# Performance work log

Measured on AMD Instinct MI355X. Metric: run time of the kernel, lower is better.

The kernel has to match this reference:

```python
import jax, jax.numpy as jnp
import numpy as np

SR = 24000          # sampling_rate
HARM = 8            # harmonic_num
DIM = HARM + 1
SINE_AMP = 0.1
NOISE_STD = 0.003
VTHR = 0.0          # voiced_threshold


def setup_inputs() -> dict:
    key = jax.random.key(0)
    k1, k2, k3, k4 = jax.random.split(key, 4)
    B, T, UPP = 16, 800, 256
    f0 = jax.random.uniform(k1, (B, T), minval=0.0, maxval=400.0)
    f0 = f0 * (jax.random.uniform(k2, (B, T)) > 0.2).astype(jnp.float32)
    rand_ini = jax.random.uniform(k3, (B, DIM)).at[:, 0].set(0.0)
    noise_z = jax.random.normal(k4, (B, T * UPP, DIM), dtype=jnp.float32)
    return {"f0": f0, "rand_ini": rand_ini, "noise_z": noise_z, "upp": UPP}


def _linear_interp_align_corners(x, upp):
    # x: [B, T, D] -> [B, T*upp, D], matches F.interpolate(mode='linear', align_corners=True)
    B, T, D = x.shape
    L = T * upp
    pos = jnp.arange(L, dtype=x.dtype) * (T - 1) / (L - 1)
    i0 = jnp.clip(jnp.floor(pos).astype(jnp.int32), 0, T - 2)
    frac = (pos - i0.astype(x.dtype))[None, :, None]
    x0 = jnp.take(x, i0, axis=1)
    x1 = jnp.take(x, i0 + 1, axis=1)
    return x0 + frac * (x1 - x0)


def reference(f0, rand_ini, noise_z, upp):
    B, T = f0.shape
    dt = f0.dtype
    # harmonic stack: f0_buf[:, :, k] = f0 * (k+1)
    harmonics = jnp.arange(1, DIM + 1, dtype=dt)
    f0_buf = f0[:, :, None] * harmonics                      # [B, T, DIM]
    rad = (f0_buf / SR) % 1.0                                # normalized phase increments
    rad = rad.at[:, 0, :].add(rand_ini)                      # random initial phase (col 0 fixed)
    # phase-wrap detection via upsampled cumulative phase
    tmp = jnp.cumsum(rad, axis=1) * upp
    tmp = _linear_interp_align_corners(tmp, upp)             # [B, L, DIM]
    rad_up = jnp.repeat(rad, upp, axis=1)                    # nearest upsample [B, L, DIM]
    tmp = tmp % 1.0
    wrap = (tmp[:, 1:, :] - tmp[:, :-1, :]) < 0
    shift = jnp.concatenate(
        [jnp.zeros((B, 1, DIM), dt), -wrap.astype(dt)], axis=1
    )
    sine_waves = jnp.sin(jnp.cumsum(rad_up + shift, axis=1) * (2.0 * np.pi)) * SINE_AMP
    # voiced/unvoiced mask, nearest upsampled
    uv = (f0 > VTHR).astype(dt)[:, :, None]                  # [B, T, 1]
    uv = jnp.repeat(uv, upp, axis=1)                         # [B, L, 1]
    noise_amp = uv * NOISE_STD + (1.0 - uv) * (SINE_AMP / 3.0)
    noise = noise_amp * noise_z
    sine_waves = sine_waves * uv + noise
    return (sine_waves, uv, noise)
```

## Files before the change

kernel.cpp:

```cpp
#include <hip/hip_runtime.h>

#define DIMH 9
#define FR8 8

typedef float f4 __attribute__((ext_vector_type(4)));
typedef float f2 __attribute__((ext_vector_type(2)));

__global__ __launch_bounds__(256) void scan_kernel(
    const float* __restrict__ f0, const float* __restrict__ rand_ini,
    float* __restrict__ Pf, int B, int T, int upp)
{
    int bk = blockIdx.x;
    int b = bk / DIMH;
    int k = bk - b * DIMH;
    int tid = threadIdx.x;
    float hk = (float)(k + 1);

    int t0 = tid * 4;
    f4 fv = {0.f, 0.f, 0.f, 0.f};
    if (t0 < T) fv = *(const f4*)(f0 + (size_t)b * T + t0);

    double s[4];
    double run = 0.0;
    #pragma unroll
    for (int j = 0; j < 4; ++j) {
        float x = fv[j] * hk * (1.0f / 24000.0f);
        float rad = x - truncf(x);
        if (t0 == 0 && j == 0) rad += rand_ini[b * DIMH + k];
        run += (double)rad;
        s[j] = run;
    }

    double tot = run;
    int lane = tid & 63;
    #pragma unroll
    for (int d = 1; d < 64; d <<= 1) {
        double u = __shfl_up(tot, d);
        if (lane >= d) tot += u;
    }
    __shared__ double wsum[4];
    int wid = tid >> 6;
    if (lane == 63) wsum[wid] = tot;
    __syncthreads();
    double excl = tot - run;
    for (int w = 0; w < wid; ++w) excl += wsum[w];

    if (t0 < T) {
        f4 o;
        double du = (double)upp;
        #pragma unroll
        for (int j = 0; j < 4; ++j) {
            double up = (excl + s[j]) * du;
            o[j] = (float)(up - (double)(long long)up);
        }
        *(f4*)(Pf + ((size_t)bk) * (size_t)T + t0) = o;
    }
}

template <int UPP>
__global__ __launch_bounds__(512) void sine_kernel_t(
    const float* __restrict__ f0, const float* __restrict__ rand_ini,
    const float* __restrict__ noise_z, const float* __restrict__ Pf,
    float* __restrict__ out, int B, int T)
{
    int nfb = T / FR8;
    int gb = blockIdx.x;
    int b = gb / nfb;
    int t0 = (gb - b * nfb) * FR8;
    int tid = threadIdx.x;

    __shared__ f2 srp[FR8 * DIMH];
    __shared__ float suv[FR8], snamp[FR8];

    if (tid < FR8 * DIMH) {
        int tl = tid / DIMH;
        int k  = tid - tl * DIMH;
        int t  = t0 + tl;
        float f0v = f0[(size_t)b * T + t];
        float x = f0v * (float)(k + 1) * (1.0f / 24000.0f);
        float rad = x - truncf(x);
        if (t == 0) rad += rand_ini[b * DIMH + k];
        f2 v;
        v.x = rad;
        v.y = (t > 0) ? Pf[((size_t)b * DIMH + k) * T + (t - 1)] : 0.0f;
        srp[tid] = v;
        if (k == 0) {
            float uv = (f0v > 0.0f) ? 1.0f : 0.0f;
            suv[tl] = uv;
            snamp[tl] = uv * 0.003f + (1.0f - uv) * (0.1f / 3.0f);
        }
    }
    __syncthreads();

    size_t L = (size_t)T * (size_t)UPP;
    float* out_sine  = out;
    float* out_uv    = out + (size_t)B * L * DIMH;
    float* out_noise = out_uv + (size_t)B * L;

    {
        int f = tid >> 6;
        float u = suv[f];
        f4 uvv = {u, u, u, u};
        f4* uvp = (f4*)(out_uv + (size_t)b * L + (size_t)t0 * UPP);
        uvp[tid] = uvv;
    }

    size_t base = ((size_t)b * L + (size_t)t0 * UPP) * DIMH;
    const f4* nzp = (const f4*)(noise_z + base);
    f4* sp = (f4*)(out_sine + base);
    f4* np = (f4*)(out_noise + base);

    constexpr int NIT = FR8 * UPP * DIMH / 4 / 512;
    #pragma unroll
    for (int it = 0; it < NIT; ++it) {
        int v  = tid + it * 512;
        int e0 = v << 2;
        int s  = e0 / DIMH;
        int k  = e0 - s * DIMH;
        int fidx = s / UPP;
        int rr   = s - fidx * UPP;
        float uv   = suv[fidx];
        float namp = snamp[fidx];
        f4 nz = __builtin_nontemporal_load(nzp + v);
        f4 sv, nov;
        #pragma unroll
        for (int j = 0; j < 4; ++j) {
            f2 rp = srp[fidx * DIMH + k];
            float C  = fmaf((float)(rr + 1), rp.x, rp.y);
            float fr = C - truncf(C);
#if __has_builtin(__builtin_amdgcn_sinf)
            float sn = __builtin_amdgcn_sinf(fr) * 0.1f;
#else
            float sn = sinf(6.283185307179586f * fr) * 0.1f;
#endif
            float no = namp * nz[j];
            sv[j]  = fmaf(sn, uv, no);
            nov[j] = no;
            if (++k == DIMH) { k = 0; ++rr; }
        }
        sp[v] = sv;
        np[v] = nov;
    }
}

__global__ __launch_bounds__(256) void sine_kernel_rt(
    const float* __restrict__ f0, const float* __restrict__ rand_ini,
    const float* __restrict__ noise_z, const float* __restrict__ Pf,
    float* __restrict__ out, int B, int T, int upp)
{
    const int FRAMES = 4;
    int nfb = T / FRAMES;
    int gb = blockIdx.x;
    int b = gb / nfb;
    int t0 = (gb - b * nfb) * FRAMES;
    int tid = threadIdx.x;

    __shared__ f2 srp[4 * DIMH];
    __shared__ float suv[4], snamp[4];

    if (tid < FRAMES * DIMH) {
        int tl = tid / DIMH;
        int k  = tid - tl * DIMH;
        int t  = t0 + tl;
        float f0v = f0[(size_t)b * T + t];
        float x = f0v * (float)(k + 1) * (1.0f / 24000.0f);
        float rad = x - truncf(x);
        if (t == 0) rad += rand_ini[b * DIMH + k];
        f2 v; v.x = rad;
        v.y = (t > 0) ? Pf[((size_t)b * DIMH + k) * T + (t - 1)] : 0.0f;
        srp[tid] = v;
        if (k == 0) {
            float uv = (f0v > 0.0f) ? 1.0f : 0.0f;
            suv[tl] = uv;
            snamp[tl] = uv * 0.003f + (1.0f - uv) * (0.1f / 3.0f);
        }
    }
    __syncthreads();

    size_t L = (size_t)T * (size_t)upp;
    float* out_sine  = out;
    float* out_uv    = out + (size_t)B * L * DIMH;
    float* out_noise = out_uv + (size_t)B * L;

    for (int i = tid; i < FRAMES * upp / 4; i += 256) {
        int f = i / (upp >> 2);
        float u = suv[f];
        f4 uvv = {u, u, u, u};
        ((f4*)(out_uv + (size_t)b * L + (size_t)t0 * upp))[i] = uvv;
    }

    size_t base = ((size_t)b * L + (size_t)t0 * upp) * DIMH;
    const f4* nzp = (const f4*)(noise_z + base);
    f4* sp = (f4*)(out_sine + base);
    f4* np = (f4*)(out_noise + base);

    int totf4 = FRAMES * upp * DIMH / 4;
    for (int v = tid; v < totf4; v += 256) {
        int e0 = v << 2;
        int s  = e0 / DIMH;
        int k  = e0 - s * DIMH;
        int fidx = s / upp;
        int rr   = s - fidx * upp;
        float uv   = suv[fidx];
        float namp = snamp[fidx];
        f4 nz = nzp[v];
        f4 sv, nov;
        #pragma unroll
        for (int j = 0; j < 4; ++j) {
            f2 rp = srp[fidx * DIMH + k];
            float C  = fmaf((float)(rr + 1), rp.x, rp.y);
            float fr = C - truncf(C);
            float sn = sinf(6.283185307179586f * fr) * 0.1f;
            float no = namp * nz[j];
            sv[j]  = fmaf(sn, uv, no);
            nov[j] = no;
            if (++k == DIMH) { k = 0; ++rr; }
        }
        sp[v] = sv;
        np[v] = nov;
    }
}

extern "C" void kernel_launch(void* const* d_in, const int* in_sizes, int n_in,
                              void* d_out, int out_size, void* d_ws, size_t ws_size,
                              hipStream_t stream) {
    const float* f0       = (const float*)d_in[0];
    const float* rand_ini = (const float*)d_in[1];
    const float* noise_z  = (const float*)d_in[2];
    float* out = (float*)d_out;

    int B = in_sizes[1] / DIMH;
    int T = in_sizes[0] / B;
    long long L = (long long)(in_sizes[2] / DIMH) / B;
    int upp = (int)(L / T);

    float* Pf = (float*)d_ws;

    scan_kernel<<<B * DIMH, 256, 0, stream>>>(f0, rand_ini, Pf, B, T, upp);
    if (upp == 256 && (T % FR8) == 0) {
        sine_kernel_t<256><<<B * (T / FR8), 512, 0, stream>>>(
            f0, rand_ini, noise_z, Pf, out, B, T);
    } else {
        sine_kernel_rt<<<B * (T / 4), 256, 0, stream>>>(
            f0, rand_ini, noise_z, Pf, out, B, T, upp);
    }
}
```

Measured before the change: 67.58 us.

## Fuse prefix-sum scan into sine kernel by recomputing per-block phase prefix

Drops the separate scan kernel on the fast path. Each block now recomputes the cumulative phase up to its starting frame by reducing f0 over all earlier frames for all 9 harmonics in double precision, then adds the partial sums within its 8 frames. This removes one kernel launch and the workspace round-trip. In exchange, every block does redundant O(T) work and double-precision reductions with two extra barriers, which is small next to the streaming work.

After: 66.93 us. Within noise of the previous version (-1.0%).

```diff
diff --git a/kernel.cpp b/kernel.cpp
--- a/kernel.cpp
+++ b/kernel.cpp
@@ -6,71 +6,51 @@
 typedef float f4 __attribute__((ext_vector_type(4)));
 typedef float f2 __attribute__((ext_vector_type(2)));
 
-__global__ __launch_bounds__(256) void scan_kernel(
+template <int UPP>
+__global__ __launch_bounds__(512) void fused_kernel_t(
     const float* __restrict__ f0, const float* __restrict__ rand_ini,
-    float* __restrict__ Pf, int B, int T, int upp)
-{
-    int bk = blockIdx.x;
-    int b = bk / DIMH;
-    int k = bk - b * DIMH;
-    int tid = threadIdx.x;
-    float hk = (float)(k + 1);
-
-    int t0 = tid * 4;
-    f4 fv = {0.f, 0.f, 0.f, 0.f};
-    if (t0 < T) fv = *(const f4*)(f0 + (size_t)b * T + t0);
-
-    double s[4];
-    double run = 0.0;
-    #pragma unroll
-    for (int j = 0; j < 4; ++j) {
-        float x = fv[j] * hk * (1.0f / 24000.0f);
-        float rad = x - truncf(x);
-        if (t0 == 0 && j == 0) rad += rand_ini[b * DIMH + k];
-        run += (double)rad;
-        s[j] = run;
-    }
-
-    double tot = run;
-    int lane = tid & 63;
-    #pragma unroll
-    for (int d = 1; d < 64; d <<= 1) {
-        double u = __shfl_up(tot, d);
-        if (lane >= d) tot += u;
-    }
-    __shared__ double wsum[4];
-    int wid = tid >> 6;
-    if (lane == 63) wsum[wid] = tot;
-    __syncthreads();
-    double excl = tot - run;
-    for (int w = 0; w < wid; ++w) excl += wsum[w];
-
-    if (t0 < T) {
-        f4 o;
-        double du = (double)upp;
-        #pragma unroll
-        for (int j = 0; j < 4; ++j) {
-            double up = (excl + s[j]) * du;
-            o[j] = (float)(up - (double)(long long)up);
-        }
-        *(f4*)(Pf + ((size_t)bk) * (size_t)T + t0) = o;
-    }
-}
-
-template <int UPP>
-__global__ __launch_bounds__(512) void sine_kernel_t(
-    const float* __restrict__ f0, const float* __restrict__ rand_ini,
-    const float* __restrict__ noise_z, const float* __restrict__ Pf,
-    float* __restrict__ out, int B, int T)
+    const float* __restrict__ noise_z, float* __restrict__ out, int B, int T)
 {
     int nfb = T / FR8;
     int gb = blockIdx.x;
     int b = gb / nfb;
     int t0 = (gb - b * nfb) * FR8;
     int tid = threadIdx.x;
-
+    int wid = tid >> 6, lane = tid & 63;
+
+    __shared__ double partial[8][DIMH];
+    __shared__ double sP[DIMH];
     __shared__ f2 srp[FR8 * DIMH];
     __shared__ float suv[FR8], snamp[FR8];
+
+    double acc[DIMH];
+    #pragma unroll
+    for (int k = 0; k < DIMH; ++k) acc[k] = 0.0;
+    for (int t = tid; t < t0; t += 512) {
+        float f0v = f0[(size_t)b * T + t];
+        #pragma unroll
+        for (int k = 0; k < DIMH; ++k) {
+            float x = f0v * (float)(k + 1) * (1.0f / 24000.0f);
+            float rad = x - truncf(x);
+            if (t == 0) rad += rand_ini[b * DIMH + k];
+            acc[k] += (double)rad;
+        }
+    }
+    #pragma unroll
+    for (int k = 0; k < DIMH; ++k) {
+        double a = acc[k];
+        #pragma unroll
+        for (int d = 32; d > 0; d >>= 1) a += __shfl_down(a, d);
+        if (lane == 0) partial[wid][k] = a;
+    }
+    __syncthreads();
+    if (tid < DIMH) {
+        double s = 0.0;
+        #pragma unroll
+        for (int w = 0; w < 8; ++w) s += partial[w][tid];
+        sP[tid] = s;
+    }
+    __syncthreads();
 
     if (tid < FR8 * DIMH) {
         int tl = tid / DIMH;
@@ -80,9 +60,19 @@
         float x = f0v * (float)(k + 1) * (1.0f / 24000.0f);
         float rad = x - truncf(x);
         if (t == 0) rad += rand_ini[b * DIMH + k];
+
+        double prev = sP[k];
+        for (int j = 0; j < tl; ++j) {
+            float fj = f0[(size_t)b * T + t0 + j];
+            float xj = fj * (float)(k + 1) * (1.0f / 24000.0f);
+            float rj = xj - truncf(xj);
+            if (t0 + j == 0) rj += rand_ini[b * DIMH + k];
+            prev += (double)rj;
+        }
+        double up = prev * (double)UPP;
         f2 v;
         v.x = rad;
-        v.y = (t > 0) ? Pf[((size_t)b * DIMH + k) * T + (t - 1)] : 0.0f;
+        v.y = (float)(up - (double)(long long)up);
         srp[tid] = v;
         if (k == 0) {
             float uv = (f0v > 0.0f) ? 1.0f : 0.0f;
@@ -140,6 +130,56 @@
         }
         sp[v] = sv;
         np[v] = nov;
+    }
+}
+
+__global__ __launch_bounds__(256) void scan_kernel(
+    const float* __restrict__ f0, const float* __restrict__ rand_ini,
+    float* __restrict__ Pf, int B, int T, int upp)
+{
+    int bk = blockIdx.x;
+    int b = bk / DIMH;
+    int k = bk - b * DIMH;
+    int tid = threadIdx.x;
+    float hk = (float)(k + 1);
+
+    int t0 = tid * 4;
+    f4 fv = {0.f, 0.f, 0.f, 0.f};
+    if (t0 < T) fv = *(const f4*)(f0 + (size_t)b * T + t0);
+
+    double s[4];
+    double run = 0.0;
+    #pragma unroll
+    for (int j = 0; j < 4; ++j) {
+        float x = fv[j] * hk * (1.0f / 24000.0f);
+        float rad = x - truncf(x);
+        if (t0 == 0 && j == 0) rad += rand_ini[b * DIMH + k];
+        run += (double)rad;
+        s[j] = run;
+    }
+    double tot = run;
+    int lane = tid & 63;
+    #pragma unroll
+    for (int d = 1; d < 64; d <<= 1) {
+        double u = __shfl_up(tot, d);
+        if (lane >= d) tot += u;
+    }
+    __shared__ double wsum[4];
+    int wid = tid >> 6;
+    if (lane == 63) wsum[wid] = tot;
+    __syncthreads();
+    double excl = tot - run;
+    for (int w = 0; w < wid; ++w) excl += wsum[w];
+
+    if (t0 < T) {
+        f4 o;
+        double du = (double)upp;
+        #pragma unroll
+        for (int j = 0; j < 4; ++j) {
+            double up = (excl + s[j]) * du;
+            o[j] = (float)(up - (double)(long long)up);
+        }
+        *(f4*)(Pf + ((size_t)bk) * (size_t)T + t0) = o;
     }
 }
 
@@ -234,13 +274,12 @@
     long long L = (long long)(in_sizes[2] / DIMH) / B;
     int upp = (int)(L / T);
 
-    float* Pf = (float*)d_ws;
-
-    scan_kernel<<<B * DIMH, 256, 0, stream>>>(f0, rand_ini, Pf, B, T, upp);
     if (upp == 256 && (T % FR8) == 0) {
-        sine_kernel_t<256><<<B * (T / FR8), 512, 0, stream>>>(
-            f0, rand_ini, noise_z, Pf, out, B, T);
+        fused_kernel_t<256><<<B * (T / FR8), 512, 0, stream>>>(
+            f0, rand_ini, noise_z, out, B, T);
     } else {
+        float* Pf = (float*)d_ws;
+        scan_kernel<<<B * DIMH, 256, 0, stream>>>(f0, rand_ini, Pf, B, T, upp);
         sine_kernel_rt<<<B * (T / 4), 256, 0, stream>>>(
             f0, rand_ini, noise_z, Pf, out, B, T, upp);
     }
```
